# Kernel optimization log

Measured on AMD Instinct MI355X. Metric: run time of the kernel, lower is better.

## Reference

```python
import jax, jax.numpy as jnp
import numpy as np

K = 3
PAD = 1
STRIDE = 1


def _conv2d(x, w, b):
    out = jax.lax.conv_general_dilated(
        x, w, window_strides=(STRIDE, STRIDE),
        padding=[(PAD, PAD), (PAD, PAD)],
        dimension_numbers=("NCHW", "OIHW", "NCHW"))
    return out + b[None, :, None, None]


def setup_inputs() -> dict:
    key = jax.random.key(0)
    ks = jax.random.split(key, 6)
    B, C, H, W, O = 4, 64, 128, 128, 64
    x = jax.random.normal(ks[0], (B, C, H, W), dtype=jnp.float32)
    # small-scale offset/modulator weights so sampled offsets stay O(1) pixels
    offset_w = jax.random.normal(ks[1], (2 * K * K, C, K, K), dtype=jnp.float32) * 0.02
    offset_b = jax.random.normal(ks[2], (2 * K * K,), dtype=jnp.float32) * 0.02
    mod_w = jax.random.normal(ks[3], (K * K, C, K, K), dtype=jnp.float32) * 0.02
    mod_b = jax.random.normal(ks[4], (K * K,), dtype=jnp.float32) * 0.02
    weight = jax.random.normal(ks[5], (O, C, K, K), dtype=jnp.float32) * 0.05
    return {"x": x, "offset_w": offset_w, "offset_b": offset_b,
            "mod_w": mod_w, "mod_b": mod_b, "weight": weight}


def _deform_conv(x, offset, mask, weight):
    # torchvision deform_conv2d v2 semantics, zero padding outside the image.
    B, C, H, W = x.shape
    K2 = K * K
    Ho, Wo = offset.shape[2], offset.shape[3]
    dy = offset[:, 0::2]  # [B,K2,Ho,Wo] vertical offsets
    dx = offset[:, 1::2]  # [B,K2,Ho,Wo] horizontal offsets
    ky = jnp.repeat(jnp.arange(K), K).astype(x.dtype)   # kernel row per tap
    kx = jnp.tile(jnp.arange(K), K).astype(x.dtype)     # kernel col per tap
    oy = (jnp.arange(Ho) * STRIDE - PAD).astype(x.dtype)
    ox = (jnp.arange(Wo) * STRIDE - PAD).astype(x.dtype)
    py = oy[None, None, :, None] + ky[None, :, None, None] + dy  # [B,K2,Ho,Wo]
    px = ox[None, None, None, :] + kx[None, :, None, None] + dx

    y0 = jnp.floor(py)
    x0 = jnp.floor(px)
    wy1 = py - y0  # bilinear weights toward the +1 corner
    wx1 = px - x0
    y0i = y0.astype(jnp.int32)
    x0i = x0.astype(jnp.int32)

    xf = x.reshape(B, C, H * W)

    def gather(yc, xc, wgt):
        valid = ((yc >= 0) & (yc < H) & (xc >= 0) & (xc < W)).astype(x.dtype)
        idx = jnp.clip(yc, 0, H - 1) * W + jnp.clip(xc, 0, W - 1)  # [B,K2,Ho,Wo]
        flat = idx.reshape(B, 1, -1)
        g = jnp.take_along_axis(xf, jnp.broadcast_to(flat, (B, C, flat.shape[-1])), axis=2)
        g = g.reshape(B, C, K2, Ho, Wo)
        return g * (wgt * valid)[:, None]

    samp = (gather(y0i,     x0i,     (1 - wy1) * (1 - wx1))
            + gather(y0i,     x0i + 1, (1 - wy1) * wx1)
            + gather(y0i + 1, x0i,     wy1 * (1 - wx1))
            + gather(y0i + 1, x0i + 1, wy1 * wx1))  # [B,C,K2,Ho,Wo]

    wr = weight.reshape(weight.shape[0], C, K2)
    return jnp.einsum("ock,bckhw->bohw", wr, samp * mask[:, None])


def reference(x, offset_w, offset_b, mod_w, mod_b, weight):
    offset = _conv2d(x, offset_w, offset_b)
    mask = 2.0 * jax.nn.sigmoid(_conv2d(x, mod_w, mod_b))
    return _deform_conv(x, offset, mask, weight)
```

## Files before the change

kernel.cpp:

```cpp
#include <hip/hip_runtime.h>
#include <hip/hip_bf16.h>
#include <math.h>

typedef unsigned short u16;
typedef unsigned int   u32;
typedef __attribute__((ext_vector_type(8))) short short8;
typedef __attribute__((ext_vector_type(4))) float f32x4;

#define B_  4
#define C_  64
#define H_  128
#define W_  128
#define O_  64
#define HW_ (H_ * W_)

__device__ __forceinline__ u16 f2bf(float f) {
    __hip_bfloat16 h = __float2bfloat16(f);
    u16 u; __builtin_memcpy(&u, &h, 2); return u;
}
__device__ __forceinline__ float bf2f(u16 u) {
    return __uint_as_float((u32)u << 16);
}
__device__ __forceinline__ u32 pkbf(float lo, float hi) {
    return ((u32)f2bf(hi) << 16) | (u32)f2bf(lo);
}
__device__ __forceinline__ float bflo(u32 v) { return __uint_as_float(v << 16); }
__device__ __forceinline__ float bfhi(u32 v) { return __uint_as_float(v & 0xffff0000u); }

__device__ __forceinline__ uint4 interp8(
    uint4 c00, uint4 c01, uint4 c10, uint4 c11,
    float wtx, float wty, float wtz, float wtw)
{
    const u32* q00 = (const u32*)&c00;
    const u32* q01 = (const u32*)&c01;
    const u32* q10 = (const u32*)&c10;
    const u32* q11 = (const u32*)&c11;
    u32 bw[4];
#pragma unroll
    for (int q = 0; q < 4; ++q) {
        float slo = bflo(q00[q]) * wtx;
        slo = fmaf(bflo(q01[q]), wty, slo);
        slo = fmaf(bflo(q10[q]), wtz, slo);
        slo = fmaf(bflo(q11[q]), wtw, slo);
        float shi = bfhi(q00[q]) * wtx;
        shi = fmaf(bfhi(q01[q]), wty, shi);
        shi = fmaf(bfhi(q10[q]), wtz, shi);
        shi = fmaf(bfhi(q11[q]), wtw, shi);
        bw[q] = pkbf(slo, shi);
    }
    uint4 v; __builtin_memcpy(&v, bw, 16);
    return v;
}

__global__ __launch_bounds__(256) void prep(
    const float* __restrict__ x, const float* __restrict__ weight,
    const float* __restrict__ ow, const float* __restrict__ mw,
    u16* __restrict__ xt, u16* __restrict__ Wb, u16* __restrict__ OWb)
{
    int i = blockIdx.x, t = threadIdx.x;
    if (i < 1024) {
        __shared__ float tile[64][65];
        int lb = i >> 8;
        int pix0 = (i & 255) << 6;
        const float* xb = x + ((size_t)lb << 20);
#pragma unroll
        for (int it = 0; it < 4; ++it) {
            int e = it * 256 + t;
            int c = e >> 4;
            int pl4 = (e & 15) << 2;
            float4 v = *(const float4*)&xb[((size_t)c << 14) + pix0 + pl4];
            tile[c][pl4 + 0] = v.x;
            tile[c][pl4 + 1] = v.y;
            tile[c][pl4 + 2] = v.z;
            tile[c][pl4 + 3] = v.w;
        }
        __syncthreads();
        u16* xo = xt + ((((size_t)lb << 14) + pix0) << 6);
#pragma unroll
        for (int it = 0; it < 4; ++it) {
            int e = it * 256 + t;
            int c4 = (e & 15) << 2;
            int pl = e >> 4;
            ushort4 v;
            v.x = f2bf(tile[c4 + 0][pl]);
            v.y = f2bf(tile[c4 + 1][pl]);
            v.z = f2bf(tile[c4 + 2][pl]);
            v.w = f2bf(tile[c4 + 3][pl]);
            *(ushort4*)&xo[((size_t)pl << 6) + c4] = v;
        }
    } else {
        int e = (i - 1024) * 256 + t;
        if (e < 36864) {
            int j = e & 7, ln = (e >> 3) & 63;
            int ks = (e >> 9) % 18, ot = e / 9216;
            int o = ot * 16 + (ln & 15);
            int kidx = ks * 32 + ((ln >> 4) << 3) + j;
            int k = kidx >> 6, c = kidx & 63;
            Wb[e] = f2bf(weight[((size_t)(o * 64 + c)) * 9 + k]);
        } else {
            int e2 = e - 36864;
            int j = e2 & 7, ln = (e2 >> 3) & 63;
            int ks = (e2 >> 9) % 18, ot = e2 / 9216;
            int o = ot * 16 + (ln & 15);
            int kidx = ks * 32 + ((ln >> 4) << 3) + j;
            int k = kidx >> 6, c = kidx & 63;
            float v = 0.0f;
            if (o < 18)      v = ow[((size_t)(o * 64 + c)) * 9 + k];
            else if (o < 27) v = mw[((size_t)((o - 18) * 64 + c)) * 9 + k];
            OWb[e2] = f2bf(v);
        }
    }
}

__global__ __launch_bounds__(256, 7) void fused_dcn(
    const u16* __restrict__ xt,
    const u16* __restrict__ Wb, const u16* __restrict__ OWb,
    const float* __restrict__ ob, const float* __restrict__ mb,
    float* __restrict__ out)
{
    __shared__ __align__(16) u16 S[16][576];
    __shared__ float   param[27][16];
    __shared__ __align__(8) ushort4 pwp[144];
    __shared__ __align__(8) ushort4 pww[144];

    const int t = threadIdx.x;
    const int lane = t & 63;
    const int wv = t >> 6;

    int bid0 = blockIdx.x;
    const int bid = (bid0 & 7) * 512 + (bid0 >> 3);
    const int lb = bid >> 10;
    const int pix0 = (bid & 1023) << 4;
    const int h  = pix0 >> 7;
    const int w0 = pix0 & 127;

    const u16* xtb = xt + ((size_t)lb << 20);
    const char* xb8 = (const char*)xtb;

#pragma unroll
    for (int i = 0; i < 4; ++i) {
        int e = i * 256 + t;
        int u = e >> 3, oct = e & 7;
        int k = u >> 4, pixl = u & 15;
        int ky = k / 3, kx = k - 3 * ky;
        int y = h - 1 + ky, xx = w0 + pixl - 1 + kx;
        bool valid = ((unsigned)y < 128u) && ((unsigned)xx < 128u);
        int idx = ((y & 127) << 7) + (xx & 127);
        uint4 v = *(const uint4*)(xtb + ((size_t)idx << 6) + (oct << 3));
        v.x = valid ? v.x : 0u;
        v.y = valid ? v.y : 0u;
        v.z = valid ? v.z : 0u;
        v.w = valid ? v.w : 0u;
        *(uint4*)&S[pixl][k * 64 + ((oct ^ (pixl & 7)) << 3)] = v;
    }
    if (t < 128) {
        int e = 1024 + t;
        int u = e >> 3, oct = e & 7;
        int pixl = u & 15;
        int y = h + 1;
        int xx = w0 + pixl - 1 + 2;
        bool valid = ((unsigned)y < 128u) && ((unsigned)xx < 128u);
        int idx = ((y & 127) << 7) + (xx & 127);
        uint4 v = *(const uint4*)(xtb + ((size_t)idx << 6) + (oct << 3));
        v.x = valid ? v.x : 0u;
        v.y = valid ? v.y : 0u;
        v.z = valid ? v.z : 0u;
        v.w = valid ? v.w : 0u;
        *(uint4*)&S[pixl][8 * 64 + ((oct ^ (pixl & 7)) << 3)] = v;
    }
    __syncthreads();

    if (wv < 2) {
        f32x4 k1a = {0.f, 0.f, 0.f, 0.f};
        f32x4 k1b = {0.f, 0.f, 0.f, 0.f};
        int brow = lane & 15;
        int hi = lane >> 4;
        int swz = (brow & 7) << 3;
#pragma unroll
        for (int kp = 0; kp < 9; ++kp) {
            int ks0 = kp * 2, ks1 = kp * 2 + 1;
            short8 a0 = ((const short8*)OWb)[(wv * 18 + ks0) * 64 + lane];
            short8 a1 = ((const short8*)OWb)[(wv * 18 + ks1) * 64 + lane];
            short8 b0 = *(const short8*)&S[brow][kp * 64 + ((hi << 3) ^ swz)];
            short8 b1 = *(const short8*)&S[brow][kp * 64 + ((32 + (hi << 3)) ^ swz)];
            k1a = __builtin_amdgcn_mfma_f32_16x16x32_bf16(a0, b0, k1a, 0, 0, 0);
            k1b = __builtin_amdgcn_mfma_f32_16x16x32_bf16(a1, b1, k1b, 0, 0, 0);
        }
#pragma unroll
        for (int r = 0; r < 4; ++r) {
            int oc = wv * 16 + (hi << 2) + r;
            float v = k1a[r] + k1b[r];
            if (oc < 18) {
                param[oc][brow] = v + ob[oc];
            } else if (oc < 27) {
                float s = v + mb[oc - 18];
                param[oc][brow] = 2.0f / (1.0f + __expf(-s));
            }
        }
    }
    __syncthreads();

    if (t < 144) {
        int tap = t >> 4, pixl = t & 15;
        int ky = tap / 3, kx = tap - 3 * ky;
        float dy = param[2 * tap][pixl];
        float dx = param[2 * tap + 1][pixl];
        float m  = param[18 + tap][pixl];
        float py = (float)(h - 1 + ky) + dy;
        float px = (float)(w0 + pixl - 1 + kx) + dx;
        float y0f = floorf(py), x0f = floorf(px);
        float fy = py - y0f, fx = px - x0f;
        int y0 = (int)y0f, x0 = (int)x0f;
        int y1 = y0 + 1, x1 = x0 + 1;
        bool vy0 = (unsigned)y0 < (unsigned)H_;
        bool vy1 = (unsigned)y1 < (unsigned)H_;
        bool vx0 = (unsigned)x0 < (unsigned)W_;
        bool vx1 = (unsigned)x1 < (unsigned)W_;
        float w00 = (1.f - fy) * (1.f - fx) * m; if (!(vy0 && vx0)) w00 = 0.f;
        float w01 = (1.f - fy) * fx          * m; if (!(vy0 && vx1)) w01 = 0.f;
        float w10 = fy * (1.f - fx)          * m; if (!(vy1 && vx0)) w10 = 0.f;
        float w11 = fy * fx                   * m; if (!(vy1 && vx1)) w11 = 0.f;
        int y0c = min(max(y0, 0), H_ - 1);
        int y1c = min(max(y1, 0), H_ - 1);
        int x0c = min(max(x0, 0), W_ - 1);
        int x1c = min(max(x1, 0), W_ - 1);
        pwp[t] = make_ushort4((u16)((y0c << 7) + x0c), (u16)((y0c << 7) + x1c),
                              (u16)((y1c << 7) + x0c), (u16)((y1c << 7) + x1c));
        pww[t] = make_ushort4(f2bf(w00), f2bf(w01), f2bf(w10), f2bf(w11));
    }
    __syncthreads();

#pragma unroll
    for (int ii = 0; ii < 2; ++ii) {
        int e0 = ii * 512 + t;
        int e1 = e0 + 256;
        int u0 = e0 >> 3, o0 = e0 & 7;
        int u1 = e1 >> 3, o1 = e1 & 7;
        ushort4 pp0 = pwp[u0]; ushort4 wq0 = pww[u0];
        ushort4 pp1 = pwp[u1]; ushort4 wq1 = pww[u1];
        int co0 = o0 << 4, co1 = o1 << 4;
        uint4 a00 = *(const uint4*)(xb8 + ((int)pp0.x << 7) + co0);
        uint4 a01 = *(const uint4*)(xb8 + ((int)pp0.y << 7) + co0);
        uint4 a10 = *(const uint4*)(xb8 + ((int)pp0.z << 7) + co0);
        uint4 a11 = *(const uint4*)(xb8 + ((int)pp0.w << 7) + co0);
        uint4 b00 = *(const uint4*)(xb8 + ((int)pp1.x << 7) + co1);
        uint4 b01 = *(const uint4*)(xb8 + ((int)pp1.y << 7) + co1);
        uint4 b10 = *(const uint4*)(xb8 + ((int)pp1.z << 7) + co1);
        uint4 b11 = *(const uint4*)(xb8 + ((int)pp1.w << 7) + co1);
        __builtin_amdgcn_sched_barrier(0);
        {
            int k = u0 >> 4, pixl = u0 & 15;
            uint4 v = interp8(a00, a01, a10, a11,
                              bf2f(wq0.x), bf2f(wq0.y), bf2f(wq0.z), bf2f(wq0.w));
            *(uint4*)&S[pixl][k * 64 + ((o0 ^ (pixl & 7)) << 3)] = v;
        }
        {
            int k = u1 >> 4, pixl = u1 & 15;
            uint4 v = interp8(b00, b01, b10, b11,
                              bf2f(wq1.x), bf2f(wq1.y), bf2f(wq1.z), bf2f(wq1.w));
            *(uint4*)&S[pixl][k * 64 + ((o1 ^ (pixl & 7)) << 3)] = v;
        }
    }
    if (t < 128) {
        int e = 1024 + t;
        int u = e >> 3, oct = e & 7;
        int pixl = u & 15;
        ushort4 pp = pwp[u]; ushort4 wq = pww[u];
        int co = oct << 4;
        uint4 c00 = *(const uint4*)(xb8 + ((int)pp.x << 7) + co);
        uint4 c01 = *(const uint4*)(xb8 + ((int)pp.y << 7) + co);
        uint4 c10 = *(const uint4*)(xb8 + ((int)pp.z << 7) + co);
        uint4 c11 = *(const uint4*)(xb8 + ((int)pp.w << 7) + co);
        uint4 v = interp8(c00, c01, c10, c11,
                          bf2f(wq.x), bf2f(wq.y), bf2f(wq.z), bf2f(wq.w));
        *(uint4*)&S[pixl][8 * 64 + ((oct ^ (pixl & 7)) << 3)] = v;
    }
    __syncthreads();

    {
        f32x4 acca = {0.f, 0.f, 0.f, 0.f};
        f32x4 accb = {0.f, 0.f, 0.f, 0.f};
        int brow = lane & 15;
        int hi = lane >> 4;
        int swz = (brow & 7) << 3;
#pragma unroll
        for (int kp = 0; kp < 9; ++kp) {
            int ks0 = kp * 2, ks1 = kp * 2 + 1;
            short8 b0 = *(const short8*)&S[brow][kp * 64 + ((hi << 3) ^ swz)];
            short8 b1 = *(const short8*)&S[brow][kp * 64 + ((32 + (hi << 3)) ^ swz)];
            short8 a0 = ((const short8*)Wb)[(wv * 18 + ks0) * 64 + lane];
            short8 a1 = ((const short8*)Wb)[(wv * 18 + ks1) * 64 + lane];
            acca = __builtin_amdgcn_mfma_f32_16x16x32_bf16(a0, b0, acca, 0, 0, 0);
            accb = __builtin_amdgcn_mfma_f32_16x16x32_bf16(a1, b1, accb, 0, 0, 0);
        }
        float* op = out + ((size_t)lb << 20) + pix0;
#pragma unroll
        for (int r = 0; r < 4; ++r) {
            int o = wv * 16 + (hi << 2) + r;
            op[((size_t)o << 14) + brow] = acca[r] + accb[r];
        }
    }
}

extern "C" void kernel_launch(void* const* d_in, const int* in_sizes, int n_in,
                              void* d_out, int out_size, void* d_ws, size_t ws_size,
                              hipStream_t stream)
{
    const float* x        = (const float*)d_in[0];
    const float* offset_w = (const float*)d_in[1];
    const float* offset_b = (const float*)d_in[2];
    const float* mod_w    = (const float*)d_in[3];
    const float* mod_b    = (const float*)d_in[4];
    const float* weight   = (const float*)d_in[5];
    float* out = (float*)d_out;

    u16* Wb  = (u16*)d_ws;
    u16* OWb = Wb + 36864;
    u16* xt  = OWb + 18432;

    prep<<<1240, 256, 0, stream>>>(x, weight, offset_w, mod_w, xt, Wb, OWb);
    fused_dcn<<<4096, 256, 0, stream>>>(xt, Wb, OWb, offset_b, mod_b, out);
}
```

Measured before the change: 44.29 us.

## Split fused kernel into offset-conv and deform-conv kernels via packed sample buffer

Splits the single fused kernel into a conv_off kernel, which computes offsets and masks with MFMA using operands loaded straight from global memory, and a dcn kernel that reads the packed sample indices and weights from a workspace buffer. The aim is to remove the LDS staging and the extra barriers of the offset stage, and to let each stage run at its own occupancy: 128 threads per block for conv_off, 256 threads with a higher launch bound for dcn. The cost is an extra kernel launch and a 9 MB global round trip for the packed parameters.

```diff
diff --git a/kernel.cpp b/kernel.cpp
--- a/kernel.cpp
+++ b/kernel.cpp
@@ -17,9 +17,6 @@
 __device__ __forceinline__ u16 f2bf(float f) {
     __hip_bfloat16 h = __float2bfloat16(f);
     u16 u; __builtin_memcpy(&u, &h, 2); return u;
-}
-__device__ __forceinline__ float bf2f(u16 u) {
-    return __uint_as_float((u32)u << 16);
 }
 __device__ __forceinline__ u32 pkbf(float lo, float hi) {
     return ((u32)f2bf(hi) << 16) | (u32)f2bf(lo);
@@ -112,20 +109,18 @@
     }
 }
 
-__global__ __launch_bounds__(256, 7) void fused_dcn(
-    const u16* __restrict__ xt,
-    const u16* __restrict__ Wb, const u16* __restrict__ OWb,
+__global__ __launch_bounds__(128, 6) void conv_off(
+    const u16* __restrict__ xt, const u16* __restrict__ OWb,
     const float* __restrict__ ob, const float* __restrict__ mb,
-    float* __restrict__ out)
-{
-    __shared__ __align__(16) u16 S[16][576];
-    __shared__ float   param[27][16];
-    __shared__ __align__(8) ushort4 pwp[144];
-    __shared__ __align__(8) ushort4 pww[144];
+    uint4* __restrict__ pk)
+{
+    __shared__ float param[27][16];
 
     const int t = threadIdx.x;
     const int lane = t & 63;
     const int wv = t >> 6;
+    const int mypix = lane & 15;
+    const int hi = lane >> 4;
 
     int bid0 = blockIdx.x;
     const int bid = (bid0 & 7) * 512 + (bid0 >> 3);
@@ -135,73 +130,60 @@
     const int w0 = pix0 & 127;
 
     const u16* xtb = xt + ((size_t)lb << 20);
-    const char* xb8 = (const char*)xtb;
-
-#pragma unroll
-    for (int i = 0; i < 4; ++i) {
-        int e = i * 256 + t;
-        int u = e >> 3, oct = e & 7;
-        int k = u >> 4, pixl = u & 15;
-        int ky = k / 3, kx = k - 3 * ky;
-        int y = h - 1 + ky, xx = w0 + pixl - 1 + kx;
-        bool valid = ((unsigned)y < 128u) && ((unsigned)xx < 128u);
-        int idx = ((y & 127) << 7) + (xx & 127);
-        uint4 v = *(const uint4*)(xtb + ((size_t)idx << 6) + (oct << 3));
-        v.x = valid ? v.x : 0u;
-        v.y = valid ? v.y : 0u;
-        v.z = valid ? v.z : 0u;
-        v.w = valid ? v.w : 0u;
-        *(uint4*)&S[pixl][k * 64 + ((oct ^ (pixl & 7)) << 3)] = v;
-    }
-    if (t < 128) {
-        int e = 1024 + t;
-        int u = e >> 3, oct = e & 7;
-        int pixl = u & 15;
-        int y = h + 1;
-        int xx = w0 + pixl - 1 + 2;
-        bool valid = ((unsigned)y < 128u) && ((unsigned)xx < 128u);
-        int idx = ((y & 127) << 7) + (xx & 127);
-        uint4 v = *(const uint4*)(xtb + ((size_t)idx << 6) + (oct << 3));
-        v.x = valid ? v.x : 0u;
-        v.y = valid ? v.y : 0u;
-        v.z = valid ? v.z : 0u;
-        v.w = valid ? v.w : 0u;
-        *(uint4*)&S[pixl][8 * 64 + ((oct ^ (pixl & 7)) << 3)] = v;
+
+    f32x4 k1a = {0.f, 0.f, 0.f, 0.f};
+    f32x4 k1b = {0.f, 0.f, 0.f, 0.f};
+#pragma unroll
+    for (int half = 0; half < 2; ++half) {
+        uint4 raw[9];
+#pragma unroll
+        for (int q = 0; q < 9; ++q) {
+            int ks = half * 9 + q;
+            int tap = ks >> 1;
+            int ky = tap / 3, kx = tap - 3 * ky;
+            int y  = h - 1 + ky;
+            int xx = w0 + mypix - 1 + kx;
+            int idx = ((y & 127) << 7) + (xx & 127);
+            raw[q] = *(const uint4*)(xtb + ((size_t)idx << 6) + ((ks & 1) << 5) + (hi << 3));
+        }
+        __builtin_amdgcn_sched_barrier(0);
+#pragma unroll
+        for (int q = 0; q < 9; ++q) {
+            int ks = half * 9 + q;
+            int tap = ks >> 1;
+            int ky = tap / 3, kx = tap - 3 * ky;
+            int y  = h - 1 + ky;
+            int xx = w0 + mypix - 1 + kx;
+            bool valid = ((unsigned)y < 128u) && ((unsigned)xx < 128u);
+            uint4 rw = raw[q];
+            rw.x = valid ? rw.x : 0u;
+            rw.y = valid ? rw.y : 0u;
+            rw.z = valid ? rw.z : 0u;
+            rw.w = valid ? rw.w : 0u;
+            short8 bfr;
+            __builtin_memcpy(&bfr, &rw, 16);
+            short8 wa = ((const short8*)OWb)[(wv * 18 + ks) * 64 + lane];
+            if (half == 0)
+                k1a = __builtin_amdgcn_mfma_f32_16x16x32_bf16(wa, bfr, k1a, 0, 0, 0);
+            else
+                k1b = __builtin_amdgcn_mfma_f32_16x16x32_bf16(wa, bfr, k1b, 0, 0, 0);
+        }
+    }
+#pragma unroll
+    for (int r = 0; r < 4; ++r) {
+        int oc = (wv << 4) + (hi << 2) + r;
+        float v = k1a[r] + k1b[r];
+        if (oc < 18) {
+            param[oc][mypix] = v + ob[oc];
+        } else if (oc < 27) {
+            float s = v + mb[oc - 18];
+            param[oc][mypix] = 2.0f / (1.0f + __expf(-s));
+        }
     }
     __syncthreads();
 
-    if (wv < 2) {
-        f32x4 k1a = {0.f, 0.f, 0.f, 0.f};
-        f32x4 k1b = {0.f, 0.f, 0.f, 0.f};
-        int brow = lane & 15;
-        int hi = lane >> 4;
-        int swz = (brow & 7) << 3;
-#pragma unroll
-        for (int kp = 0; kp < 9; ++kp) {
-            int ks0 = kp * 2, ks1 = kp * 2 + 1;
-            short8 a0 = ((const short8*)OWb)[(wv * 18 + ks0) * 64 + lane];
-            short8 a1 = ((const short8*)OWb)[(wv * 18 + ks1) * 64 + lane];
-            short8 b0 = *(const short8*)&S[brow][kp * 64 + ((hi << 3) ^ swz)];
-            short8 b1 = *(const short8*)&S[brow][kp * 64 + ((32 + (hi << 3)) ^ swz)];
-            k1a = __builtin_amdgcn_mfma_f32_16x16x32_bf16(a0, b0, k1a, 0, 0, 0);
-            k1b = __builtin_amdgcn_mfma_f32_16x16x32_bf16(a1, b1, k1b, 0, 0, 0);
-        }
-#pragma unroll
-        for (int r = 0; r < 4; ++r) {
-            int oc = wv * 16 + (hi << 2) + r;
-            float v = k1a[r] + k1b[r];
-            if (oc < 18) {
-                param[oc][brow] = v + ob[oc];
-            } else if (oc < 27) {
-                float s = v + mb[oc - 18];
-                param[oc][brow] = 2.0f / (1.0f + __expf(-s));
-            }
-        }
-    }
-    __syncthreads();
-
-    if (t < 144) {
-        int tap = t >> 4, pixl = t & 15;
+    for (int p = t; p < 144; p += 128) {
+        int tap = p >> 4, pixl = p & 15;
         int ky = tap / 3, kx = tap - 3 * ky;
         float dy = param[2 * tap][pixl];
         float dx = param[2 * tap + 1][pixl];
@@ -224,11 +206,32 @@
         int y1c = min(max(y1, 0), H_ - 1);
         int x0c = min(max(x0, 0), W_ - 1);
         int x1c = min(max(x1, 0), W_ - 1);
-        pwp[t] = make_ushort4((u16)((y0c << 7) + x0c), (u16)((y0c << 7) + x1c),
-                              (u16)((y1c << 7) + x0c), (u16)((y1c << 7) + x1c));
-        pww[t] = make_ushort4(f2bf(w00), f2bf(w01), f2bf(w10), f2bf(w11));
-    }
-    __syncthreads();
+        pk[(size_t)bid * 144 + p] = make_uint4(
+            (u32)((y0c << 7) + x0c) | ((u32)((y0c << 7) + x1c) << 16),
+            (u32)((y1c << 7) + x0c) | ((u32)((y1c << 7) + x1c) << 16),
+            (u32)f2bf(w00) | ((u32)f2bf(w01) << 16),
+            (u32)f2bf(w10) | ((u32)f2bf(w11) << 16));
+    }
+}
+
+__global__ __launch_bounds__(256, 8) void dcn(
+    const u16* __restrict__ xt, const u16* __restrict__ Wb,
+    const uint4* __restrict__ pk, float* __restrict__ out)
+{
+    __shared__ __align__(16) u16 S[16][576];
+
+    const int t = threadIdx.x;
+    const int lane = t & 63;
+    const int wv = t >> 6;
+
+    int bid0 = blockIdx.x;
+    const int bid = (bid0 & 7) * 512 + (bid0 >> 3);
+    const int lb = bid >> 10;
+    const int pix0 = (bid & 1023) << 4;
+
+    const u16* xtb = xt + ((size_t)lb << 20);
+    const char* xb8 = (const char*)xtb;
+    const uint4* pkb = pk + (size_t)bid * 144;
 
 #pragma unroll
     for (int ii = 0; ii < 2; ++ii) {
@@ -236,28 +239,28 @@
         int e1 = e0 + 256;
         int u0 = e0 >> 3, o0 = e0 & 7;
         int u1 = e1 >> 3, o1 = e1 & 7;
-        ushort4 pp0 = pwp[u0]; ushort4 wq0 = pww[u0];
-        ushort4 pp1 = pwp[u1]; ushort4 wq1 = pww[u1];
+        uint4 q0 = pkb[u0];
+        uint4 q1 = pkb[u1];
         int co0 = o0 << 4, co1 = o1 << 4;
-        uint4 a00 = *(const uint4*)(xb8 + ((int)pp0.x << 7) + co0);
-        uint4 a01 = *(const uint4*)(xb8 + ((int)pp0.y << 7) + co0);
-        uint4 a10 = *(const uint4*)(xb8 + ((int)pp0.z << 7) + co0);
-        uint4 a11 = *(const uint4*)(xb8 + ((int)pp0.w << 7) + co0);
-        uint4 b00 = *(const uint4*)(xb8 + ((int)pp1.x << 7) + co1);
-        uint4 b01 = *(const uint4*)(xb8 + ((int)pp1.y << 7) + co1);
-        uint4 b10 = *(const uint4*)(xb8 + ((int)pp1.z << 7) + co1);
-        uint4 b11 = *(const uint4*)(xb8 + ((int)pp1.w << 7) + co1);
+        uint4 a00 = *(const uint4*)(xb8 + ((q0.x & 0xffffu) << 7) + co0);
+        uint4 a01 = *(const uint4*)(xb8 + ((q0.x >> 16) << 7) + co0);
+        uint4 a10 = *(const uint4*)(xb8 + ((q0.y & 0xffffu) << 7) + co0);
+        uint4 a11 = *(const uint4*)(xb8 + ((q0.y >> 16) << 7) + co0);
+        uint4 b00 = *(const uint4*)(xb8 + ((q1.x & 0xffffu) << 7) + co1);
+        uint4 b01 = *(const uint4*)(xb8 + ((q1.x >> 16) << 7) + co1);
+        uint4 b10 = *(const uint4*)(xb8 + ((q1.y & 0xffffu) << 7) + co1);
+        uint4 b11 = *(const uint4*)(xb8 + ((q1.y >> 16) << 7) + co1);
         __builtin_amdgcn_sched_barrier(0);
         {
             int k = u0 >> 4, pixl = u0 & 15;
             uint4 v = interp8(a00, a01, a10, a11,
-                              bf2f(wq0.x), bf2f(wq0.y), bf2f(wq0.z), bf2f(wq0.w));
+                              bflo(q0.z), bfhi(q0.z), bflo(q0.w), bfhi(q0.w));
             *(uint4*)&S[pixl][k * 64 + ((o0 ^ (pixl & 7)) << 3)] = v;
         }
         {
             int k = u1 >> 4, pixl = u1 & 15;
             uint4 v = interp8(b00, b01, b10, b11,
-                              bf2f(wq1.x), bf2f(wq1.y), bf2f(wq1.z), bf2f(wq1.w));
+                              bflo(q1.z), bfhi(q1.z), bflo(q1.w), bfhi(q1.w));
             *(uint4*)&S[pixl][k * 64 + ((o1 ^ (pixl & 7)) << 3)] = v;
         }
     }
@@ -265,14 +268,14 @@
         int e = 1024 + t;
         int u = e >> 3, oct = e & 7;
         int pixl = u & 15;
-        ushort4 pp = pwp[u]; ushort4 wq = pww[u];
+        uint4 q = pkb[u];
         int co = oct << 4;
-        uint4 c00 = *(const uint4*)(xb8 + ((int)pp.x << 7) + co);
-        uint4 c01 = *(const uint4*)(xb8 + ((int)pp.y << 7) + co);
-        uint4 c10 = *(const uint4*)(xb8 + ((int)pp.z << 7) + co);
-        uint4 c11 = *(const uint4*)(xb8 + ((int)pp.w << 7) + co);
+        uint4 c00 = *(const uint4*)(xb8 + ((q.x & 0xffffu) << 7) + co);
+        uint4 c01 = *(const uint4*)(xb8 + ((q.x >> 16) << 7) + co);
+        uint4 c10 = *(const uint4*)(xb8 + ((q.y & 0xffffu) << 7) + co);
+        uint4 c11 = *(const uint4*)(xb8 + ((q.y >> 16) << 7) + co);
         uint4 v = interp8(c00, c01, c10, c11,
-                          bf2f(wq.x), bf2f(wq.y), bf2f(wq.z), bf2f(wq.w));
+                          bflo(q.z), bfhi(q.z), bflo(q.w), bfhi(q.w));
         *(uint4*)&S[pixl][8 * 64 + ((oct ^ (pixl & 7)) << 3)] = v;
     }
     __syncthreads();
@@ -314,10 +317,12 @@
     const float* weight   = (const float*)d_in[5];
     float* out = (float*)d_out;
 
-    u16* Wb  = (u16*)d_ws;
+    uint4* pk = (uint4*)d_ws;
+    u16* Wb  = (u16*)((char*)d_ws + 9437184);
     u16* OWb = Wb + 36864;
     u16* xt  = OWb + 18432;
 
     prep<<<1240, 256, 0, stream>>>(x, weight, offset_w, mod_w, xt, Wb, OWb);
-    fused_dcn<<<4096, 256, 0, stream>>>(xt, Wb, OWb, offset_b, mod_b, out);
-}
+    conv_off<<<4096, 128, 0, stream>>>(xt, OWb, offset_b, mod_b, pk);
+    dcn<<<4096, 256, 0, stream>>>(xt, Wb, pk, out);
+}
```

New measurement: 61.65 us. 39.2% more time.
